# Kernel tuning notes

Measured on AMD Instinct MI355X. Metric: run time of the kernel, lower is better.

The kernel has to match this reference:

```python
import jax, jax.numpy as jnp
import numpy as np
import math

FRACTION = 1.0 / math.e  # GOLDEN_ZONE_CENTER


def setup_inputs() -> dict:
    key = jax.random.key(0)
    x = jax.random.normal(key, (4, 4096, 2048), dtype=jnp.float32)
    return {"x": x}


def reference(x) -> jnp.ndarray:
    # Training-mode forward of BoltzmannGateSTE: keep only top-k (k = n/e)
    # activations by global magnitude, zero the rest.
    flat = jnp.abs(x).reshape(-1)
    n = flat.shape[0]
    k = max(1, int(n * FRACTION))  # static python int -> jit-friendly
    if k >= n:
        return x
    topk_vals, _ = jax.lax.top_k(flat, k)
    threshold = topk_vals[-1]  # k-th largest magnitude
    mask = (jnp.abs(x) >= threshold).astype(x.dtype)
    return x * mask
```

## Files before the change

### kernel.cpp

```cpp
#include <hip/hip_runtime.h>
#include <stdint.h>
#include <string.h>


#define SEL_T 1024
constexpr int SEL_W = SEL_T / 64;

constexpr unsigned LO_BITS = 0x3F6147AEu;
constexpr unsigned HI_BITS = 0x3F6B851Fu;
constexpr unsigned NKEY    = HI_BITS - LO_BITS;
constexpr int      NCB     = (NKEY + 1023) / 1024;

constexpr int P_GRID = 4096;
constexpr int P_BLK  = 256;
constexpr int P_WPB  = P_BLK / 64;
constexpr int NWAVES = P_GRID * P_WPB;
constexpr int CAPW   = 128;

constexpr int NBIN1   = 4096;
constexpr int NFINE   = 1 << 19;
constexpr int NCOARSE = 512;
constexpr int F_GRID  = 256;
constexpr int F_BLK   = 256;

#define S_PREF 0
#define S_K1   1
#define S_T    2
#define S_FLAG 3

__device__ __forceinline__ bool gate_skip(const unsigned* state, int gate) {
    if (gate == 0) return false;
    unsigned fl = state[S_FLAG];
    return (gate == 1) ? (fl == 0u) : (fl != 0u);
}

__global__ __launch_bounds__(P_BLK, 8)
void pass_partition(const uint4* __restrict__ x, long long n4,
                    uint4* __restrict__ out, uint2* __restrict__ cand,
                    unsigned* __restrict__ wavecnt, unsigned* __restrict__ blkchi,
                    unsigned* __restrict__ fineH, unsigned* __restrict__ state)
{
    typedef unsigned uv4 __attribute__((ext_vector_type(4)));
    const int lane  = threadIdx.x & 63;
    const int wid   = threadIdx.x >> 6;
    const int gwave = blockIdx.x * P_WPB + wid;
    uint2* my = cand + (size_t)gwave * CAPW;
    const unsigned long long lt = (1ull << lane) - 1ull;

    unsigned wcnt = 0;
    unsigned chi  = 0;
    const long long stride = (long long)gridDim.x * P_BLK;
#pragma unroll 2
    for (long long i = (long long)blockIdx.x * P_BLK + threadIdx.x; i < n4; i += stride) {
        uint4 v = x[i];
        uint4 r;
        unsigned idx0 = (unsigned)(i << 2);
#define DO_COMP(c, off)                                                        \
        { unsigned b = v.c, u = b & 0x7FFFFFFFu;                               \
          bool kp = (u >= HI_BITS);                                            \
          bool cd = (u >= LO_BITS) & !kp;                                      \
          chi += (unsigned)kp;                                                 \
          r.c = kp ? b : 0u;                                                   \
          unsigned long long m = __ballot(cd);                                 \
          if (cd) {                                                            \
              atomicAdd(&fineH[u - LO_BITS], 1u);         \
              unsigned pos = wcnt + (unsigned)__popcll(m & lt);                \
              if (pos < (unsigned)CAPW) my[pos] = make_uint2(b, idx0 + off);   \
          }                                                                    \
          wcnt += (unsigned)__popcll(m); }
        DO_COMP(x, 0) DO_COMP(y, 1) DO_COMP(z, 2) DO_COMP(w, 3)
#undef DO_COMP
        __builtin_nontemporal_store(*(uv4*)&r, (uv4*)(out + i));
    }

    for (int m = 32; m; m >>= 1) chi += __shfl_xor(chi, m, 64);
    __shared__ unsigned s_chi[P_WPB];
    if (lane == 0) {
        s_chi[wid] = chi;
        wavecnt[gwave] = (wcnt < (unsigned)CAPW) ? wcnt : (unsigned)CAPW;
        if (wcnt > (unsigned)CAPW) atomicOr(&state[S_FLAG], 1u);
    }
    __syncthreads();
    if (threadIdx.x == 0) {
        unsigned a = 0;
        for (int w = 0; w < P_WPB; ++w) a += s_chi[w];
        blkchi[blockIdx.x] = a;
    }
}

__global__ __launch_bounds__(64)
void coarse_reduce(const unsigned* __restrict__ fineH, unsigned* __restrict__ coarseH)
{
    unsigned base = blockIdx.x << 10;
    unsigned s = 0;
    for (int t = threadIdx.x; t < 1024; t += 64) {
        unsigned key = base + t;
        s += (key < NKEY) ? fineH[key] : 0u;
    }
    for (int m = 32; m; m >>= 1) s += __shfl_xor(s, m, 64);
    if (threadIdx.x == 0) coarseH[blockIdx.x] = s;
}

__device__ void select_desc(const unsigned* __restrict__ hist, int nbins,
                            unsigned k, unsigned* s_wsum, int* s_res)
{
    const int tid  = threadIdx.x;
    const int lane = tid & 63;
    const int wid  = tid >> 6;
    if (tid == 0) { s_res[0] = -1; s_res[1] = 0; }
    __syncthreads();
    unsigned running = 0;
    for (int top = nbins; top > 0; top -= SEL_T) {
        int bin = top - 1 - tid;
        unsigned v = (bin >= 0) ? hist[bin] : 0u;
        unsigned p = v;
#pragma unroll
        for (int off = 1; off < 64; off <<= 1) {
            unsigned t = __shfl_up(p, off, 64);
            if (lane >= off) p += t;
        }
        if (lane == 63) s_wsum[wid] = p;
        __syncthreads();
        unsigned wpref = 0, total = 0;
#pragma unroll
        for (int w = 0; w < SEL_W; ++w) {
            unsigned ws = s_wsum[w];
            wpref += (w < wid) ? ws : 0u;
            total += ws;
        }
        unsigned incl = wpref + p;
        unsigned excl = incl - v;
        if (running + total >= k) {
            if (bin >= 0 && running + incl >= k && running + excl < k) {
                s_res[0] = bin;
                s_res[1] = (int)(k - running - excl);
            }
            __syncthreads();
            return;
        }
        running += total;
        __syncthreads();
    }
    __syncthreads();
}

__global__ __launch_bounds__(SEL_T)
void fast_select(const unsigned* __restrict__ blkchi, const unsigned* __restrict__ wavecnt,
                 const unsigned* __restrict__ coarseH, const unsigned* __restrict__ fineH,
                 unsigned* __restrict__ state, unsigned k)
{
    if (state[S_FLAG]) return;
    __shared__ unsigned s_wsum[SEL_W];
    __shared__ int s_res[2];
    __shared__ unsigned long long s_red[SEL_W][2];
    __shared__ unsigned s_kp;
    __shared__ int s_bad;

    unsigned long long chi = 0, tot = 0;
    for (int i = threadIdx.x; i < P_GRID; i += SEL_T) chi += blkchi[i];
    for (int i = threadIdx.x; i < NWAVES; i += SEL_T) tot += wavecnt[i];
    for (int m = 32; m; m >>= 1) {
        chi += __shfl_xor(chi, m, 64);
        tot += __shfl_xor(tot, m, 64);
    }
    int wid = threadIdx.x >> 6, lane = threadIdx.x & 63;
    if (lane == 0) { s_red[wid][0] = chi; s_red[wid][1] = tot; }
    __syncthreads();
    if (threadIdx.x == 0) {
        unsigned long long C = 0, Tt = 0;
        for (int w = 0; w < SEL_W; ++w) { C += s_red[w][0]; Tt += s_red[w][1]; }
        if (C >= (unsigned long long)k || C + Tt < (unsigned long long)k) {
            state[S_FLAG] = 1u;
            s_bad = 1;
        } else { s_bad = 0; s_kp = (unsigned)((unsigned long long)k - C); }
    }
    __syncthreads();
    if (s_bad) return;
    unsigned kp = s_kp;

    select_desc(coarseH, NCB, kp, s_wsum, s_res);
    int cb      = s_res[0];
    unsigned r  = (unsigned)s_res[1];
    __syncthreads();
    int nfine = (int)NKEY - cb * 1024;
    if (nfine > 1024) nfine = 1024;
    select_desc(fineH + (size_t)cb * 1024, nfine, r, s_wsum, s_res);
    int f = s_res[0];
    if (threadIdx.x == 0)
        state[S_T] = LO_BITS + (unsigned)(cb * 1024 + f);
}

__global__ __launch_bounds__(256)
void cand_fixup(const uint2* __restrict__ cand, const unsigned* __restrict__ state,
                float* __restrict__ out, long long n)
{
    if (state[S_FLAG]) return;
    unsigned T = state[S_T];
    long long total = (long long)NWAVES * CAPW;
    long long stride = (long long)gridDim.x * 256;
    for (long long j = (long long)blockIdx.x * 256 + threadIdx.x; j < total; j += stride) {
        uint2 e = cand[j];
        if ((e.x & 0x7FFFFFFFu) >= T && e.y < (unsigned long long)n)
            out[e.y] = __uint_as_float(e.x);
    }
}

__global__ __launch_bounds__(F_BLK)
void f_hist1(const uint4* __restrict__ x, long long n4, unsigned* __restrict__ histA,
             const unsigned* __restrict__ state, int gate)
{
    if (gate_skip(state, gate)) return;
    __shared__ unsigned h[NBIN1];
    for (int i = threadIdx.x; i < NBIN1; i += F_BLK) h[i] = 0u;
    __syncthreads();
    long long stride = (long long)gridDim.x * F_BLK;
    for (long long i = (long long)blockIdx.x * F_BLK + threadIdx.x; i < n4; i += stride) {
        uint4 v = x[i];
        atomicAdd(&h[(v.x & 0x7FFFFFFFu) >> 19], 1u);
        atomicAdd(&h[(v.y & 0x7FFFFFFFu) >> 19], 1u);
        atomicAdd(&h[(v.z & 0x7FFFFFFFu) >> 19], 1u);
        atomicAdd(&h[(v.w & 0x7FFFFFFFu) >> 19], 1u);
    }
    __syncthreads();
    for (int i = threadIdx.x; i < NBIN1; i += F_BLK)
        if (h[i]) atomicAdd(&histA[i], h[i]);
}

__global__ __launch_bounds__(SEL_T)
void f_select1(const unsigned* __restrict__ histA, unsigned* __restrict__ state,
               unsigned k, int gate)
{
    if (gate_skip(state, gate)) return;
    __shared__ unsigned s_wsum[SEL_W];
    __shared__ int s_res[2];
    select_desc(histA, NBIN1, k, s_wsum, s_res);
    if (threadIdx.x == 0) {
        state[S_PREF] = (s_res[0] < 0) ? 0u : (unsigned)s_res[0];
        state[S_K1]   = (s_res[0] < 0) ? 1u : (unsigned)s_res[1];
    }
}

__global__ __launch_bounds__(F_BLK)
void f_hist2(const uint4* __restrict__ x, long long n4, const unsigned* __restrict__ state,
             unsigned* __restrict__ fineB, unsigned* __restrict__ coarseB, int gate)
{
    if (gate_skip(state, gate)) return;
    __shared__ unsigned hc[NCOARSE];
    for (int i = threadIdx.x; i < NCOARSE; i += F_BLK) hc[i] = 0u;
    __syncthreads();
    unsigned pref = state[S_PREF];
    long long stride = (long long)gridDim.x * F_BLK;
    for (long long i = (long long)blockIdx.x * F_BLK + threadIdx.x; i < n4; i += stride) {
        uint4 v = x[i];
        unsigned u;
#define DO_C(c) u = v.c & 0x7FFFFFFFu;                                        \
        if ((u >> 19) == pref) {                                              \
            atomicAdd(&fineB[u & (NFINE - 1)], 1u);                           \
            atomicAdd(&hc[(u & (NFINE - 1)) >> 10], 1u); }
        DO_C(x) DO_C(y) DO_C(z) DO_C(w)
#undef DO_C
    }
    __syncthreads();
    for (int i = threadIdx.x; i < NCOARSE; i += F_BLK)
        if (hc[i]) atomicAdd(&coarseB[i], hc[i]);
}

__global__ __launch_bounds__(SEL_T)
void f_select2(const unsigned* __restrict__ fineB, const unsigned* __restrict__ coarseB,
               unsigned* __restrict__ state, int gate)
{
    if (gate_skip(state, gate)) return;
    __shared__ unsigned s_wsum[SEL_W];
    __shared__ int s_res[2];
    unsigned pref = state[S_PREF];
    unsigned k    = state[S_K1];
    select_desc(coarseB, NCOARSE, k, s_wsum, s_res);
    int c       = (s_res[0] < 0) ? 0 : s_res[0];
    unsigned k1 = (s_res[0] < 0) ? 1u : (unsigned)s_res[1];
    __syncthreads();
    select_desc(fineB + (size_t)c * 1024, 1024, k1, s_wsum, s_res);
    int f = (s_res[0] < 0) ? 0 : s_res[0];
    if (threadIdx.x == 0)
        state[S_T] = (pref << 19) | ((unsigned)c << 10) | (unsigned)f;
}

__global__ __launch_bounds__(256)
void f_mask(const uint4* __restrict__ x, uint4* __restrict__ out, long long n4,
            const unsigned* __restrict__ state, int gate)
{
    if (gate_skip(state, gate)) return;
    unsigned t = state[S_T];
    long long stride = (long long)gridDim.x * 256;
    for (long long i = (long long)blockIdx.x * 256 + threadIdx.x; i < n4; i += stride) {
        uint4 v = x[i];
        uint4 r;
        r.x = ((v.x & 0x7FFFFFFFu) >= t) ? v.x : 0u;
        r.y = ((v.y & 0x7FFFFFFFu) >= t) ? v.y : 0u;
        r.z = ((v.z & 0x7FFFFFFFu) >= t) ? v.z : 0u;
        r.w = ((v.w & 0x7FFFFFFFu) >= t) ? v.w : 0u;
        out[i] = r;
    }
}

extern "C" void kernel_launch(void* const* d_in, const int* in_sizes, int n_in,
                              void* d_out, int out_size, void* d_ws, size_t ws_size,
                              hipStream_t stream)
{
    long long n = (long long)in_sizes[0];
    if (n <= 0) return;
    long long n4 = n >> 2;

    const double FRACTION = 1.0 / 2.718281828459045;
    long long k = (long long)((double)n * FRACTION);
    if (k < 1) k = 1;

    const size_t off_state   = 0;
    const size_t off_fineH   = 64;
    const size_t off_coarseH = off_fineH   + (((size_t)NKEY * 4 + 63) & ~63ull);
    const size_t off_fineB   = off_coarseH + (((size_t)NCB * 4 + 63) & ~63ull);
    const size_t off_coarseB = off_fineB   + (size_t)NFINE * 4;
    const size_t off_histA   = off_coarseB + (size_t)NCOARSE * 4;
    const size_t zero_end    = off_histA   + (size_t)NBIN1 * 4;
    const size_t off_wcnt    = zero_end;
    const size_t off_bchi    = off_wcnt + (size_t)NWAVES * 4;
    const size_t off_cand    = off_bchi + (size_t)P_GRID * 4;
    const size_t need_fast   = off_cand + (size_t)NWAVES * CAPW * 8;
    const size_t need_fb     = zero_end;

    uint8_t* base;
    unsigned* state = (unsigned*)d_ws;
    bool fast;
    if (ws_size >= need_fast)     { base = (uint8_t*)d_ws;  fast = true;  }
    else if (ws_size >= need_fb)  { base = (uint8_t*)d_ws;  fast = false; }
    else                          { base = (uint8_t*)d_out; fast = false;
                                    state = (unsigned*)d_ws; }

    unsigned* fineH   = (unsigned*)(base + off_fineH);
    unsigned* coarseH = (unsigned*)(base + off_coarseH);
    unsigned* fineB   = (unsigned*)(base + off_fineB);
    unsigned* coarseB = (unsigned*)(base + off_coarseB);
    unsigned* histA   = (unsigned*)(base + off_histA);
    unsigned* wavecnt = (unsigned*)(base + off_wcnt);
    unsigned* blkchi  = (unsigned*)(base + off_bchi);
    uint2*    cand    = (uint2*)   (base + off_cand);

    const uint4* x = (const uint4*)d_in[0];

    if (fast) {
        hipMemsetAsync(base, 0, zero_end, stream);
        pass_partition<<<P_GRID, P_BLK, 0, stream>>>(x, n4, (uint4*)d_out, cand,
                                                     wavecnt, blkchi, fineH, state);
        coarse_reduce <<<NCB, 64, 0, stream>>>(fineH, coarseH);
        fast_select   <<<1, SEL_T, 0, stream>>>(blkchi, wavecnt, coarseH, fineH,
                                                state, (unsigned)k);
        cand_fixup    <<<512, 256, 0, stream>>>(cand, state, (float*)d_out, n);
        f_hist1  <<<F_GRID, F_BLK, 0, stream>>>(x, n4, histA, state, 1);
        f_select1<<<1, SEL_T, 0, stream>>>(histA, state, (unsigned)k, 1);
        f_hist2  <<<F_GRID, F_BLK, 0, stream>>>(x, n4, state, fineB, coarseB, 1);
        f_select2<<<1, SEL_T, 0, stream>>>(fineB, coarseB, state, 1);
        f_mask   <<<1024, 256, 0, stream>>>(x, (uint4*)d_out, n4, state, 1);
    } else {
        if (state == (unsigned*)d_ws && base != (uint8_t*)d_ws)
            hipMemsetAsync(state, 0, 64, stream);
        hipMemsetAsync(base + off_fineB, 0,
                       ((size_t)NFINE + NCOARSE + NBIN1) * 4, stream);
        if (base == (uint8_t*)d_ws) hipMemsetAsync(state, 0, 64, stream);
        f_hist1  <<<F_GRID, F_BLK, 0, stream>>>(x, n4, histA, state, 0);
        f_select1<<<1, SEL_T, 0, stream>>>(histA, state, (unsigned)k, 0);
        f_hist2  <<<F_GRID, F_BLK, 0, stream>>>(x, n4, state, fineB, coarseB, 0);
        f_select2<<<1, SEL_T, 0, stream>>>(fineB, coarseB, state, 0);
        f_mask   <<<1024, 256, 0, stream>>>(x, (uint4*)d_out, n4, state, 0);
    }
}
```

Before: 304.5 us.

## Fuse reduce/select stages via last-block atomic tickets to cut kernel launches

Merges the coarse-histogram reduction, count reduction and threshold selection into one kernel. The last block to finish, found with an atomic ticket counter, performs the selection. The fallback histogram and select kernels are fused in the same way, and the candidate fixup now scans only each wave's valid entries instead of the full candidate buffer. This removes several small serial launches and wasted candidate reads, at the cost of threadfence/atomic completion logic and some extra code complexity.

```diff
diff --git a/kernel.cpp b/kernel.cpp
--- a/kernel.cpp
+++ b/kernel.cpp
@@ -1,10 +1,6 @@
 #include <hip/hip_runtime.h>
 #include <stdint.h>
-#include <string.h>
-
-
-#define SEL_T 1024
-constexpr int SEL_W = SEL_T / 64;
+
 
 constexpr unsigned LO_BITS = 0x3F6147AEu;
 constexpr unsigned HI_BITS = 0x3F6B851Fu;
@@ -17,22 +13,20 @@
 constexpr int NWAVES = P_GRID * P_WPB;
 constexpr int CAPW   = 128;
 
+constexpr int TPART  = 64;
+constexpr int KCS_GRID = NCB + TPART;
+
 constexpr int NBIN1   = 4096;
 constexpr int NFINE   = 1 << 19;
 constexpr int NCOARSE = 512;
-constexpr int F_GRID  = 256;
-constexpr int F_BLK   = 256;
 
 #define S_PREF 0
 #define S_K1   1
 #define S_T    2
 #define S_FLAG 3
-
-__device__ __forceinline__ bool gate_skip(const unsigned* state, int gate) {
-    if (gate == 0) return false;
-    unsigned fl = state[S_FLAG];
-    return (gate == 1) ? (fl == 0u) : (fl != 0u);
-}
+#define S_TICK 4
+#define S_TICK2 5
+#define S_TICK3 6
 
 __global__ __launch_bounds__(P_BLK, 8)
 void pass_partition(const uint4* __restrict__ x, long long n4,
@@ -88,29 +82,49 @@
     }
 }
 
-__global__ __launch_bounds__(64)
-void coarse_reduce(const unsigned* __restrict__ fineH, unsigned* __restrict__ coarseH)
-{
-    unsigned base = blockIdx.x << 10;
-    unsigned s = 0;
-    for (int t = threadIdx.x; t < 1024; t += 64) {
-        unsigned key = base + t;
-        s += (key < NKEY) ? fineH[key] : 0u;
-    }
-    for (int m = 32; m; m >>= 1) s += __shfl_xor(s, m, 64);
-    if (threadIdx.x == 0) coarseH[blockIdx.x] = s;
-}
-
-__device__ void select_desc(const unsigned* __restrict__ hist, int nbins,
-                            unsigned k, unsigned* s_wsum, int* s_res)
-{
+__device__ __forceinline__ void select1k(const unsigned* __restrict__ hist, int nbins,
+                                         unsigned k, unsigned* s_wsum, int* s_res)
+{
+    const int tid = threadIdx.x, lane = tid & 63, wid = tid >> 6;
+    __syncthreads();
+    if (tid == 0) { s_res[0] = 0; s_res[1] = 1; }
+    int bin = nbins - 1 - tid;
+    unsigned v = (bin >= 0) ? hist[bin] : 0u;
+    unsigned p = v;
+#pragma unroll
+    for (int off = 1; off < 64; off <<= 1) {
+        unsigned t = __shfl_up(p, off, 64);
+        if (lane >= off) p += t;
+    }
+    if (lane == 63) s_wsum[wid] = p;
+    __syncthreads();
+    unsigned wpref = 0;
+#pragma unroll
+    for (int w = 0; w < 16; ++w) {
+        unsigned ws = s_wsum[w];
+        wpref += (w < wid) ? ws : 0u;
+    }
+    unsigned incl = wpref + p, excl = incl - v;
+    if (bin >= 0 && incl >= k && excl < k) {
+        s_res[0] = bin;
+        s_res[1] = (int)(k - excl);
+    }
+    __syncthreads();
+}
+
+template<int TB>
+__device__ void select_desc_t(const unsigned* __restrict__ hist, int nbins,
+                              unsigned k, unsigned* s_wsum, int* s_res)
+{
+    constexpr int TW = TB / 64;
     const int tid  = threadIdx.x;
     const int lane = tid & 63;
     const int wid  = tid >> 6;
+    __syncthreads();
     if (tid == 0) { s_res[0] = -1; s_res[1] = 0; }
     __syncthreads();
     unsigned running = 0;
-    for (int top = nbins; top > 0; top -= SEL_T) {
+    for (int top = nbins; top > 0; top -= TB) {
         int bin = top - 1 - tid;
         unsigned v = (bin >= 0) ? hist[bin] : 0u;
         unsigned p = v;
@@ -123,7 +137,7 @@
         __syncthreads();
         unsigned wpref = 0, total = 0;
 #pragma unroll
-        for (int w = 0; w < SEL_W; ++w) {
+        for (int w = 0; w < TW; ++w) {
             unsigned ws = s_wsum[w];
             wpref += (w < wid) ? ws : 0u;
             total += ws;
@@ -144,77 +158,119 @@
     __syncthreads();
 }
 
-__global__ __launch_bounds__(SEL_T)
-void fast_select(const unsigned* __restrict__ blkchi, const unsigned* __restrict__ wavecnt,
-                 const unsigned* __restrict__ coarseH, const unsigned* __restrict__ fineH,
-                 unsigned* __restrict__ state, unsigned k)
-{
-    if (state[S_FLAG]) return;
-    __shared__ unsigned s_wsum[SEL_W];
+__global__ __launch_bounds__(1024)
+void kcs(const unsigned* __restrict__ fineH,
+         const unsigned* __restrict__ blkchi, const unsigned* __restrict__ wavecnt,
+         unsigned* __restrict__ coarseH, unsigned long long* __restrict__ tpart,
+         unsigned* __restrict__ state, unsigned k)
+{
+    __shared__ unsigned s_t[16];
+    __shared__ unsigned s_wsum[16];
     __shared__ int s_res[2];
-    __shared__ unsigned long long s_red[SEL_W][2];
-    __shared__ unsigned s_kp;
-    __shared__ int s_bad;
-
-    unsigned long long chi = 0, tot = 0;
-    for (int i = threadIdx.x; i < P_GRID; i += SEL_T) chi += blkchi[i];
-    for (int i = threadIdx.x; i < NWAVES; i += SEL_T) tot += wavecnt[i];
-    for (int m = 32; m; m >>= 1) {
-        chi += __shfl_xor(chi, m, 64);
-        tot += __shfl_xor(tot, m, 64);
-    }
-    int wid = threadIdx.x >> 6, lane = threadIdx.x & 63;
-    if (lane == 0) { s_red[wid][0] = chi; s_red[wid][1] = tot; }
-    __syncthreads();
-    if (threadIdx.x == 0) {
-        unsigned long long C = 0, Tt = 0;
-        for (int w = 0; w < SEL_W; ++w) { C += s_red[w][0]; Tt += s_red[w][1]; }
-        if (C >= (unsigned long long)k || C + Tt < (unsigned long long)k) {
-            state[S_FLAG] = 1u;
-            s_bad = 1;
-        } else { s_bad = 0; s_kp = (unsigned)((unsigned long long)k - C); }
-    }
-    __syncthreads();
-    if (s_bad) return;
-    unsigned kp = s_kp;
-
-    select_desc(coarseH, NCB, kp, s_wsum, s_res);
-    int cb      = s_res[0];
-    unsigned r  = (unsigned)s_res[1];
-    __syncthreads();
-    int nfine = (int)NKEY - cb * 1024;
+    __shared__ unsigned s_ct[2];
+    __shared__ unsigned s_done;
+
+    const int tid = threadIdx.x, lane = tid & 63, wid = tid >> 6;
+    const int bid = blockIdx.x;
+
+    if (bid < NCB) {
+        unsigned key = ((unsigned)bid << 10) + (unsigned)tid;
+        unsigned s = (key < NKEY) ? fineH[key] : 0u;
+        for (int m = 32; m; m >>= 1) s += __shfl_xor(s, m, 64);
+        if (lane == 0) s_t[wid] = s;
+        __syncthreads();
+        if (tid == 0) {
+            unsigned a = 0;
+#pragma unroll
+            for (int w = 0; w < 16; ++w) a += s_t[w];
+            coarseH[bid] = a;
+        }
+    } else {
+        int b = bid - NCB;
+        unsigned chi = (tid < 64)  ? blkchi[(b << 6) + tid]  : 0u;
+        unsigned tot = (tid < 256) ? wavecnt[(b << 8) + tid] : 0u;
+        for (int m = 32; m; m >>= 1) {
+            chi += __shfl_xor(chi, m, 64);
+            tot += __shfl_xor(tot, m, 64);
+        }
+        if (lane == 0) s_t[wid] = tot;
+        __syncthreads();
+        if (tid == 0) {
+            unsigned tt = 0;
+#pragma unroll
+            for (int w = 0; w < 16; ++w) tt += s_t[w];
+            tpart[b] = ((unsigned long long)chi << 32) | (unsigned long long)tt;
+        }
+    }
+    __syncthreads();
+
+    if (tid == 0) { __threadfence(); s_done = atomicAdd(&state[S_TICK], 1u); }
+    __syncthreads();
+    if (s_done != (unsigned)(KCS_GRID - 1)) return;
+    __threadfence();
+
+    unsigned long long chiS = 0, totS = 0;
+    if (wid == 0) {
+        unsigned long long e = tpart[lane];
+        chiS = e >> 32; totS = e & 0xFFFFFFFFull;
+        for (int m = 32; m; m >>= 1) {
+            chiS += __shfl_xor(chiS, m, 64);
+            totS += __shfl_xor(totS, m, 64);
+        }
+    }
+    if (tid == 0) {
+        unsigned fl = state[S_FLAG];
+        if (fl == 0u && (chiS >= (unsigned long long)k ||
+                         chiS + totS < (unsigned long long)k)) {
+            atomicOr(&state[S_FLAG], 1u);
+            fl = 1u;
+        }
+        s_ct[0] = (fl == 0u) ? 1u : 0u;
+        s_ct[1] = (unsigned)((unsigned long long)k - chiS);
+    }
+    __syncthreads();
+    if (!s_ct[0]) return;
+    unsigned kp = s_ct[1];
+
+    select1k(coarseH, NCB, kp, s_wsum, s_res);
+    int cb = s_res[0];
+    unsigned r = (unsigned)s_res[1];
+    int nfine = (int)NKEY - (cb << 10);
     if (nfine > 1024) nfine = 1024;
-    select_desc(fineH + (size_t)cb * 1024, nfine, r, s_wsum, s_res);
-    int f = s_res[0];
-    if (threadIdx.x == 0)
-        state[S_T] = LO_BITS + (unsigned)(cb * 1024 + f);
-}
-
-__global__ __launch_bounds__(256)
-void cand_fixup(const uint2* __restrict__ cand, const unsigned* __restrict__ state,
-                float* __restrict__ out, long long n)
-{
-    if (state[S_FLAG]) return;
-    unsigned T = state[S_T];
-    long long total = (long long)NWAVES * CAPW;
+    select1k(fineH + ((size_t)cb << 10), nfine, r, s_wsum, s_res);
+    if (tid == 0)
+        state[S_T] = LO_BITS + (unsigned)((cb << 10) + s_res[0]);
+}
+
+__global__ __launch_bounds__(256, 8)
+void post1(const uint4* __restrict__ x, long long n4, long long n,
+           float* __restrict__ outF,
+           const uint2* __restrict__ cand, const unsigned* __restrict__ wavecnt,
+           unsigned* __restrict__ histA, unsigned* __restrict__ state, unsigned k)
+{
+    const int tid = threadIdx.x, lane = tid & 63, wid = tid >> 6;
+
+    if (state[S_FLAG] == 0u) {
+        unsigned T = state[S_T];
+        int gw = blockIdx.x * 4 + wid;
+        int gstride = (int)gridDim.x * 4;
+        for (int w = gw; w < NWAVES; w += gstride) {
+            unsigned cnt = wavecnt[w];
+            const uint2* my = cand + (size_t)w * CAPW;
+            for (unsigned j = (unsigned)lane; j < cnt; j += 64) {
+                uint2 e = my[j];
+                if ((e.x & 0x7FFFFFFFu) >= T && (long long)e.y < n)
+                    outF[e.y] = __uint_as_float(e.x);
+            }
+        }
+        return;
+    }
+
+    __shared__ unsigned h[NBIN1];
+    for (int i = tid; i < NBIN1; i += 256) h[i] = 0u;
+    __syncthreads();
     long long stride = (long long)gridDim.x * 256;
-    for (long long j = (long long)blockIdx.x * 256 + threadIdx.x; j < total; j += stride) {
-        uint2 e = cand[j];
-        if ((e.x & 0x7FFFFFFFu) >= T && e.y < (unsigned long long)n)
-            out[e.y] = __uint_as_float(e.x);
-    }
-}
-
-__global__ __launch_bounds__(F_BLK)
-void f_hist1(const uint4* __restrict__ x, long long n4, unsigned* __restrict__ histA,
-             const unsigned* __restrict__ state, int gate)
-{
-    if (gate_skip(state, gate)) return;
-    __shared__ unsigned h[NBIN1];
-    for (int i = threadIdx.x; i < NBIN1; i += F_BLK) h[i] = 0u;
-    __syncthreads();
-    long long stride = (long long)gridDim.x * F_BLK;
-    for (long long i = (long long)blockIdx.x * F_BLK + threadIdx.x; i < n4; i += stride) {
+    for (long long i = (long long)blockIdx.x * 256 + tid; i < n4; i += stride) {
         uint4 v = x[i];
         atomicAdd(&h[(v.x & 0x7FFFFFFFu) >> 19], 1u);
         atomicAdd(&h[(v.y & 0x7FFFFFFFu) >> 19], 1u);
@@ -222,35 +278,39 @@
         atomicAdd(&h[(v.w & 0x7FFFFFFFu) >> 19], 1u);
     }
     __syncthreads();
-    for (int i = threadIdx.x; i < NBIN1; i += F_BLK)
+    for (int i = tid; i < NBIN1; i += 256)
         if (h[i]) atomicAdd(&histA[i], h[i]);
-}
-
-__global__ __launch_bounds__(SEL_T)
-void f_select1(const unsigned* __restrict__ histA, unsigned* __restrict__ state,
-               unsigned k, int gate)
-{
-    if (gate_skip(state, gate)) return;
-    __shared__ unsigned s_wsum[SEL_W];
+    __syncthreads();
+
+    __shared__ unsigned s_done;
+    if (tid == 0) { __threadfence(); s_done = atomicAdd(&state[S_TICK2], 1u); }
+    __syncthreads();
+    if (s_done != gridDim.x - 1) return;
+    __threadfence();
+
+    __shared__ unsigned s_wsum[4];
     __shared__ int s_res[2];
-    select_desc(histA, NBIN1, k, s_wsum, s_res);
-    if (threadIdx.x == 0) {
+    select_desc_t<256>(histA, NBIN1, k, s_wsum, s_res);
+    if (tid == 0) {
         state[S_PREF] = (s_res[0] < 0) ? 0u : (unsigned)s_res[0];
         state[S_K1]   = (s_res[0] < 0) ? 1u : (unsigned)s_res[1];
     }
 }
 
-__global__ __launch_bounds__(F_BLK)
-void f_hist2(const uint4* __restrict__ x, long long n4, const unsigned* __restrict__ state,
-             unsigned* __restrict__ fineB, unsigned* __restrict__ coarseB, int gate)
-{
-    if (gate_skip(state, gate)) return;
+__global__ __launch_bounds__(256, 8)
+void post2(const uint4* __restrict__ x, long long n4,
+           unsigned* __restrict__ fineB, unsigned* __restrict__ coarseB,
+           unsigned* __restrict__ state)
+{
+    if (state[S_FLAG] == 0u) return;
+    const int tid = threadIdx.x;
+    unsigned pref = state[S_PREF];
+
     __shared__ unsigned hc[NCOARSE];
-    for (int i = threadIdx.x; i < NCOARSE; i += F_BLK) hc[i] = 0u;
-    __syncthreads();
-    unsigned pref = state[S_PREF];
-    long long stride = (long long)gridDim.x * F_BLK;
-    for (long long i = (long long)blockIdx.x * F_BLK + threadIdx.x; i < n4; i += stride) {
+    for (int i = tid; i < NCOARSE; i += 256) hc[i] = 0u;
+    __syncthreads();
+    long long stride = (long long)gridDim.x * 256;
+    for (long long i = (long long)blockIdx.x * 256 + tid; i < n4; i += stride) {
         uint4 v = x[i];
         unsigned u;
 #define DO_C(c) u = v.c & 0x7FFFFFFFu;                                        \
@@ -261,34 +321,34 @@
 #undef DO_C
     }
     __syncthreads();
-    for (int i = threadIdx.x; i < NCOARSE; i += F_BLK)
+    for (int i = tid; i < NCOARSE; i += 256)
         if (hc[i]) atomicAdd(&coarseB[i], hc[i]);
-}
-
-__global__ __launch_bounds__(SEL_T)
-void f_select2(const unsigned* __restrict__ fineB, const unsigned* __restrict__ coarseB,
-               unsigned* __restrict__ state, int gate)
-{
-    if (gate_skip(state, gate)) return;
-    __shared__ unsigned s_wsum[SEL_W];
+    __syncthreads();
+
+    __shared__ unsigned s_done;
+    if (tid == 0) { __threadfence(); s_done = atomicAdd(&state[S_TICK3], 1u); }
+    __syncthreads();
+    if (s_done != gridDim.x - 1) return;
+    __threadfence();
+
+    __shared__ unsigned s_wsum[4];
     __shared__ int s_res[2];
-    unsigned pref = state[S_PREF];
-    unsigned k    = state[S_K1];
-    select_desc(coarseB, NCOARSE, k, s_wsum, s_res);
+    unsigned k1 = state[S_K1];
+    select_desc_t<256>(coarseB, NCOARSE, k1, s_wsum, s_res);
     int c       = (s_res[0] < 0) ? 0 : s_res[0];
-    unsigned k1 = (s_res[0] < 0) ? 1u : (unsigned)s_res[1];
-    __syncthreads();
-    select_desc(fineB + (size_t)c * 1024, 1024, k1, s_wsum, s_res);
+    unsigned k2 = (s_res[0] < 0) ? 1u : (unsigned)s_res[1];
+    __syncthreads();
+    select_desc_t<256>(fineB + (size_t)c * 1024, 1024, k2, s_wsum, s_res);
     int f = (s_res[0] < 0) ? 0 : s_res[0];
-    if (threadIdx.x == 0)
+    if (tid == 0)
         state[S_T] = (pref << 19) | ((unsigned)c << 10) | (unsigned)f;
 }
 
 __global__ __launch_bounds__(256)
-void f_mask(const uint4* __restrict__ x, uint4* __restrict__ out, long long n4,
-            const unsigned* __restrict__ state, int gate)
-{
-    if (gate_skip(state, gate)) return;
+void post3(const uint4* __restrict__ x, uint4* __restrict__ out, long long n4,
+           const unsigned* __restrict__ state)
+{
+    if (state[S_FLAG] == 0u) return;
     unsigned t = state[S_T];
     long long stride = (long long)gridDim.x * 256;
     for (long long i = (long long)blockIdx.x * 256 + threadIdx.x; i < n4; i += stride) {
@@ -302,6 +362,11 @@
     }
 }
 
+__global__ void seed_flag(unsigned* state)
+{
+    if (threadIdx.x == 0) state[S_FLAG] = 1u;
+}
+
 extern "C" void kernel_launch(void* const* d_in, const int* in_sizes, int n_in,
                               void* d_out, int out_size, void* d_ws, size_t ws_size,
                               hipStream_t stream)
@@ -314,61 +379,66 @@
     long long k = (long long)((double)n * FRACTION);
     if (k < 1) k = 1;
 
-    const size_t off_state   = 0;
+    auto al = [](size_t v) { return (v + 63) & ~(size_t)63; };
+
     const size_t off_fineH   = 64;
-    const size_t off_coarseH = off_fineH   + (((size_t)NKEY * 4 + 63) & ~63ull);
-    const size_t off_fineB   = off_coarseH + (((size_t)NCB * 4 + 63) & ~63ull);
+    const size_t off_fineB   = al(off_fineH + (size_t)NKEY * 4);
     const size_t off_coarseB = off_fineB   + (size_t)NFINE * 4;
     const size_t off_histA   = off_coarseB + (size_t)NCOARSE * 4;
     const size_t zero_end    = off_histA   + (size_t)NBIN1 * 4;
-    const size_t off_wcnt    = zero_end;
-    const size_t off_bchi    = off_wcnt + (size_t)NWAVES * 4;
-    const size_t off_cand    = off_bchi + (size_t)P_GRID * 4;
+    const size_t off_coarseH = al(zero_end);
+    const size_t off_tpart   = al(off_coarseH + (size_t)NCB * 4);
+    const size_t off_wcnt    = al(off_tpart + (size_t)TPART * 8);
+    const size_t off_bchi    = al(off_wcnt + (size_t)NWAVES * 4);
+    const size_t off_cand    = al(off_bchi + (size_t)P_GRID * 4);
     const size_t need_fast   = off_cand + (size_t)NWAVES * CAPW * 8;
     const size_t need_fb     = zero_end;
 
-    uint8_t* base;
-    unsigned* state = (unsigned*)d_ws;
-    bool fast;
-    if (ws_size >= need_fast)     { base = (uint8_t*)d_ws;  fast = true;  }
-    else if (ws_size >= need_fb)  { base = (uint8_t*)d_ws;  fast = false; }
-    else                          { base = (uint8_t*)d_out; fast = false;
-                                    state = (unsigned*)d_ws; }
-
-    unsigned* fineH   = (unsigned*)(base + off_fineH);
-    unsigned* coarseH = (unsigned*)(base + off_coarseH);
-    unsigned* fineB   = (unsigned*)(base + off_fineB);
-    unsigned* coarseB = (unsigned*)(base + off_coarseB);
-    unsigned* histA   = (unsigned*)(base + off_histA);
-    unsigned* wavecnt = (unsigned*)(base + off_wcnt);
-    unsigned* blkchi  = (unsigned*)(base + off_bchi);
-    uint2*    cand    = (uint2*)   (base + off_cand);
-
     const uint4* x = (const uint4*)d_in[0];
 
-    if (fast) {
+    if (ws_size >= need_fast) {
+        uint8_t* base = (uint8_t*)d_ws;
+        unsigned* state   = (unsigned*)base;
+        unsigned* fineH   = (unsigned*)(base + off_fineH);
+        unsigned* fineB   = (unsigned*)(base + off_fineB);
+        unsigned* coarseB = (unsigned*)(base + off_coarseB);
+        unsigned* histA   = (unsigned*)(base + off_histA);
+        unsigned* coarseH = (unsigned*)(base + off_coarseH);
+        unsigned long long* tpart = (unsigned long long*)(base + off_tpart);
+        unsigned* wavecnt = (unsigned*)(base + off_wcnt);
+        unsigned* blkchi  = (unsigned*)(base + off_bchi);
+        uint2*    cand    = (uint2*)   (base + off_cand);
+
         hipMemsetAsync(base, 0, zero_end, stream);
         pass_partition<<<P_GRID, P_BLK, 0, stream>>>(x, n4, (uint4*)d_out, cand,
                                                      wavecnt, blkchi, fineH, state);
-        coarse_reduce <<<NCB, 64, 0, stream>>>(fineH, coarseH);
-        fast_select   <<<1, SEL_T, 0, stream>>>(blkchi, wavecnt, coarseH, fineH,
-                                                state, (unsigned)k);
-        cand_fixup    <<<512, 256, 0, stream>>>(cand, state, (float*)d_out, n);
-        f_hist1  <<<F_GRID, F_BLK, 0, stream>>>(x, n4, histA, state, 1);
-        f_select1<<<1, SEL_T, 0, stream>>>(histA, state, (unsigned)k, 1);
-        f_hist2  <<<F_GRID, F_BLK, 0, stream>>>(x, n4, state, fineB, coarseB, 1);
-        f_select2<<<1, SEL_T, 0, stream>>>(fineB, coarseB, state, 1);
-        f_mask   <<<1024, 256, 0, stream>>>(x, (uint4*)d_out, n4, state, 1);
+        kcs  <<<KCS_GRID, 1024, 0, stream>>>(fineH, blkchi, wavecnt, coarseH,
+                                             tpart, state, (unsigned)k);
+        post1<<<1024, 256, 0, stream>>>(x, n4, n, (float*)d_out, cand, wavecnt,
+                                        histA, state, (unsigned)k);
+        post2<<<256, 256, 0, stream>>>(x, n4, fineB, coarseB, state);
+        post3<<<1024, 256, 0, stream>>>(x, (uint4*)d_out, n4, state);
     } else {
-        if (state == (unsigned*)d_ws && base != (uint8_t*)d_ws)
+        uint8_t* base;
+        unsigned* state = (unsigned*)d_ws;
+        bool in_ws = (ws_size >= need_fb);
+        base = in_ws ? (uint8_t*)d_ws : (uint8_t*)d_out;
+        unsigned* fineB   = (unsigned*)(base + off_fineB);
+        unsigned* coarseB = (unsigned*)(base + off_coarseB);
+        unsigned* histA   = (unsigned*)(base + off_histA);
+
+        if (in_ws) {
+            hipMemsetAsync(base, 0, zero_end, stream);
+        } else {
             hipMemsetAsync(state, 0, 64, stream);
-        hipMemsetAsync(base + off_fineB, 0,
-                       ((size_t)NFINE + NCOARSE + NBIN1) * 4, stream);
-        if (base == (uint8_t*)d_ws) hipMemsetAsync(state, 0, 64, stream);
-        f_hist1  <<<F_GRID, F_BLK, 0, stream>>>(x, n4, histA, state, 0);
-        f_select1<<<1, SEL_T, 0, stream>>>(histA, state, (unsigned)k, 0);
-        f_hist2  <<<F_GRID, F_BLK, 0, stream>>>(x, n4, state, fineB, coarseB, 0);
-        f_select2<<<1, SEL_T, 0, stream>>>(fineB, coarseB, state, 0);
-        f_mask   <<<1024, 256, 0, stream>>>(x, (uint4*)d_out, n4, state, 0);
-    }
-}
+            hipMemsetAsync(base + off_fineB, 0,
+                           ((size_t)NFINE + NCOARSE + NBIN1) * 4, stream);
+        }
+        seed_flag<<<1, 64, 0, stream>>>(state);
+        post1<<<1024, 256, 0, stream>>>(x, n4, n, (float*)d_out,
+                                        (const uint2*)base, (const unsigned*)base,
+                                        histA, state, (unsigned)k);
+        post2<<<256, 256, 0, stream>>>(x, n4, fineB, coarseB, state);
+        post3<<<1024, 256, 0, stream>>>(x, (uint4*)d_out, n4, state);
+    }
+}
```

After: 298.3 us, median of 2. 1.02x faster.
